# Optimization experiments

Measured on AMD Instinct MI355X. Metric: run time of the kernel, lower is better.

Reference implementation:

```python
import jax, jax.numpy as jnp
import numpy as np

D = 512      # feature dim d
N = 8192     # context length n
LMBD = 0.9   # eligibility trace decay


def _build_consts():
    two_d1 = 2 * D + 1
    # P: single nonzero entry at bottom-right
    P = np.zeros((two_d1, two_d1), dtype=np.float32)
    P[-1, -1] = 1.0
    # M: (n+1)x(n+1); top-left n x n block is lower-triangular lmbd^(row-col),
    # last row and last column are all zero (M[-1,-1] set to 0 in torch code)
    i = np.arange(N)
    diff = i[:, None] - i[None, :]
    Mnn = np.where(diff >= 0, LMBD ** np.maximum(diff, 0), 0.0).astype(np.float32)
    M = np.zeros((N + 1, N + 1), dtype=np.float32)
    M[:N, :N] = Mnn
    # Q: top-left 2d x 2d block = [[-I, I], [0, 0]]
    I = np.eye(D, dtype=np.float32)
    Q = np.zeros((two_d1, two_d1), dtype=np.float32)
    Q[:D, :D] = -I
    Q[:D, D:2 * D] = I
    return jnp.asarray(P), jnp.asarray(M), jnp.asarray(Q)


def setup_inputs() -> dict:
    key = jax.random.key(0)
    kz, = jax.random.split(key, 1)
    Z = jax.random.normal(kz, (2 * D + 1, N + 1), dtype=jnp.float32)
    alpha = jnp.ones((1,), dtype=jnp.float32)  # learned parameter
    P, M, Q = _build_consts()
    return {"Z": Z, "alpha": alpha, "P": P, "M": M, "Q": Q}


def reference(Z, alpha, P, M, Q):
    # Z: (2d+1, n+1). Matches torch: Z + alpha/n * P @ Z @ M @ Z.T @ Q @ Z
    n = Z.shape[1] - 1
    upd = ((((P @ Z) @ M) @ Z.T) @ Q) @ Z  # left-to-right like torch's @ chain
    return Z + (alpha[0] / n) * upd
```

## Files before the change

kernel.cpp:

```cpp
#include <hip/hip_runtime.h>

#define ND   512
#define NN   8192
#define NP1  8193

typedef float f4 __attribute__((ext_vector_type(4)));

#define NWB   512

__device__ __forceinline__ int sw(int j) { return j + (j >> 5); }
#define ZSLEN 8448

__global__ __launch_bounds__(256) void kW(const float* __restrict__ Z,
                                          float* __restrict__ w,
                                          float* __restrict__ out) {
    const int b = blockIdx.x;
    const int t = threadIdx.x;

    if (b < NWB) {
        __shared__ float zs[ZSLEN];
        __shared__ float es[256];
        __shared__ float red[4];
        const int c = b;
        const size_t base = (size_t)c * NP1;
        const int pre = (4 - (c & 3)) & 3;
        const int nq  = (NP1 - pre) >> 2;

        const f4* __restrict__ src = (const f4*)(Z + base + pre);
        f4* __restrict__ dst = (f4*)(out + base + pre);

        f4 xv[8];
#pragma unroll
        for (int m = 0; m < 8; ++m) {
            int i = t + 256 * m;
            xv[m] = (i < nq) ? src[i] : (f4){0.f, 0.f, 0.f, 0.f};
        }
#pragma unroll
        for (int m = 0; m < 8; ++m) {
            int i = t + 256 * m;
            if (i < nq) __builtin_nontemporal_store(xv[m], &dst[i]);
        }
#pragma unroll
        for (int m = 0; m < 8; ++m) {
            int i = t + 256 * m;
            if (i < nq) {
                int j = pre + 4 * i;
#pragma unroll
                for (int e = 0; e < 4; ++e)
                    if (j + e < NN) zs[sw(j + e)] = xv[m][e];
            }
        }
        if (t == 0) {
            for (int e = 0; e < pre; ++e) {
                float zv = Z[base + e];
                __builtin_nontemporal_store(zv, &out[base + e]);
                zs[sw(e)] = zv;
            }
            for (int j = pre + 4 * nq; j < NP1; ++j) {
                float zv = Z[base + j];
                __builtin_nontemporal_store(zv, &out[base + j]);
                if (j < NN) zs[sw(j)] = zv;
            }
        }
        __syncthreads();

        float r[32];
#pragma unroll
        for (int i = 0; i < 32; ++i) r[i] = zs[sw(32 * t + i)];

        const float L1 = 0.9f;
        float e = r[0];
#pragma unroll
        for (int i = 1; i < 32; ++i) e = fmaf(L1, e, r[i]);
        es[t] = e;
        __syncthreads();

        const float l2 = L1 * L1, l4v = l2 * l2, l8 = l4v * l4v;
        const float l16 = l8 * l8, lam32 = l16 * l16;
        float C = 0.f;
#pragma unroll
        for (int k = 7; k >= 1; --k) {
            float ek = (t - k >= 0) ? es[t - k] : 0.f;
            C = fmaf(lam32, C, ek);
        }

        float qv = C;
#pragma unroll
        for (int i = 0; i < 32; ++i) {
            qv = fmaf(L1, qv, r[i]);
            zs[sw(32 * t + i)] = qv;
        }
        __syncthreads();

        const f4* __restrict__ zrow4 = (const f4*)(Z + (size_t)(2 * ND) * NP1);
        float a0 = 0.f, a1 = 0.f, a2 = 0.f, a3 = 0.f;
#pragma unroll
        for (int m = 0; m < 8; ++m) {
            int i = t + 256 * m;
            f4 zv = zrow4[i];
            int j = 4 * i;
            a0 = fmaf(zv[0], zs[sw(j)],     a0);
            a1 = fmaf(zv[1], zs[sw(j + 1)], a1);
            a2 = fmaf(zv[2], zs[sw(j + 2)], a2);
            a3 = fmaf(zv[3], zs[sw(j + 3)], a3);
        }
        float acc = (a0 + a1) + (a2 + a3);

        for (int off = 32; off > 0; off >>= 1)
            acc += __shfl_down(acc, off, 64);
        if ((t & 63) == 0) red[t >> 6] = acc;
        __syncthreads();
        if (t == 0) w[c] = (red[0] + red[1]) + (red[2] + red[3]);
    } else {
        const size_t ZROW = (size_t)(2 * ND) * NP1;
        const f4* __restrict__ src = (const f4*)(Z + ZROW);
        f4* __restrict__ dst = (f4*)(out + ZROW);
        int i = (b - NWB) * 256 + t;
        dst[i] = src[i];
        if (b == NWB && t == 0) out[ZROW + NN] = Z[ZROW + NN];
    }
}

__global__ __launch_bounds__(256) void kU(const float* __restrict__ Z,
                                          const float* __restrict__ w,
                                          const float* __restrict__ alpha,
                                          float* __restrict__ out) {
    int j = blockIdx.x * 256 + threadIdx.x;
    if (j >= NP1) return;
    int c0 = blockIdx.y * 16;
    const size_t DS = (size_t)ND * NP1;
    float acc0 = 0.f, acc1 = 0.f;
#pragma unroll
    for (int cb = 0; cb < 16; cb += 4) {
        int c = c0 + cb;
        size_t base = (size_t)c * NP1 + (size_t)j;
        float lo0 = Z[base          ], lo1 = Z[base +     NP1];
        float lo2 = Z[base + 2 * NP1], lo3 = Z[base + 3 * NP1];
        float hi0 = Z[base + DS          ], hi1 = Z[base + DS +     NP1];
        float hi2 = Z[base + DS + 2 * NP1], hi3 = Z[base + DS + 3 * NP1];
        __builtin_nontemporal_store(hi0, &out[base + DS          ]);
        __builtin_nontemporal_store(hi1, &out[base + DS +     NP1]);
        __builtin_nontemporal_store(hi2, &out[base + DS + 2 * NP1]);
        __builtin_nontemporal_store(hi3, &out[base + DS + 3 * NP1]);
        acc0 = fmaf(w[c],     hi0 - lo0, acc0);
        acc1 = fmaf(w[c + 1], hi1 - lo1, acc1);
        acc0 = fmaf(w[c + 2], hi2 - lo2, acc0);
        acc1 = fmaf(w[c + 3], hi3 - lo3, acc1);
    }
    float s = alpha[0] * (1.0f / (float)NN);
    atomicAdd(&out[(size_t)(2 * ND) * NP1 + j], s * (acc0 + acc1));
}

extern "C" void kernel_launch(void* const* d_in, const int* in_sizes, int n_in,
                              void* d_out, int out_size, void* d_ws, size_t ws_size,
                              hipStream_t stream) {
    const float* Z     = (const float*)d_in[0];
    const float* alpha = (const float*)d_in[1];
    float* out = (float*)d_out;

    float* w = (float*)d_ws;

    kW<<<NWB + 8, 256, 0, stream>>>(Z, w, out);
    kU<<<dim3(33, 32), 256, 0, stream>>>(Z, w, alpha, out);
}
```

Measured before the change: 23.11 us.

## Split each row's decayed-scan into two half-row blocks with carry-in term

Each row's weighted prefix-scan dot product is now split across two blocks, each covering half the columns. This doubles the block count to 1024 and halves LDS use per block. The second-half block rebuilds the carry-in from the first half by summing the last 192 elements of that half with decay weights, truncating the geometric series. kU then adds the two partial weights per row. The changes should raise occupancy and parallelism in the first kernel, at the cost of a small approximation and some redundant reads.

```diff
diff --git a/kernel.cpp b/kernel.cpp
--- a/kernel.cpp
+++ b/kernel.cpp
@@ -6,103 +6,125 @@
 
 typedef float f4 __attribute__((ext_vector_type(4)));
 
-#define NWB   512
+#define NHB  1024
 
 __device__ __forceinline__ int sw(int j) { return j + (j >> 5); }
-#define ZSLEN 8448
+#define ZSLEN 4224
+
+#define LAM16 0.18530201888518410f
+#define L64   1.1790184577738583e-3f
+#define L128  1.3900845237714559e-6f
 
 __global__ __launch_bounds__(256) void kW(const float* __restrict__ Z,
-                                          float* __restrict__ w,
+                                          float* __restrict__ w2,
                                           float* __restrict__ out) {
     const int b = blockIdx.x;
     const int t = threadIdx.x;
 
-    if (b < NWB) {
+    if (b < NHB) {
         __shared__ float zs[ZSLEN];
         __shared__ float es[256];
         __shared__ float red[4];
-        const int c = b;
-        const size_t base = (size_t)c * NP1;
+        __shared__ float Esh;
+        const int c = b >> 1, h = b & 1;
+        const size_t rbase = (size_t)c * NP1;
+        const size_t cbase = rbase + (size_t)(4096 * h);
         const int pre = (4 - (c & 3)) & 3;
-        const int nq  = (NP1 - pre) >> 2;
+        const int ncols = h ? 4097 : 4096;
+        const int nq = (ncols - pre) >> 2;
 
-        const f4* __restrict__ src = (const f4*)(Z + base + pre);
-        f4* __restrict__ dst = (f4*)(out + base + pre);
+        const f4* __restrict__ src = (const f4*)(Z + cbase + pre);
+        f4* __restrict__ dst = (f4*)(out + cbase + pre);
 
-        f4 xv[8];
+        f4 xv[4];
 #pragma unroll
-        for (int m = 0; m < 8; ++m) {
+        for (int m = 0; m < 4; ++m) {
             int i = t + 256 * m;
             xv[m] = (i < nq) ? src[i] : (f4){0.f, 0.f, 0.f, 0.f};
         }
 #pragma unroll
-        for (int m = 0; m < 8; ++m) {
+        for (int m = 0; m < 4; ++m) {
             int i = t + 256 * m;
             if (i < nq) __builtin_nontemporal_store(xv[m], &dst[i]);
         }
 #pragma unroll
-        for (int m = 0; m < 8; ++m) {
+        for (int m = 0; m < 4; ++m) {
             int i = t + 256 * m;
             if (i < nq) {
-                int j = pre + 4 * i;
+                int L = pre + 4 * i;
 #pragma unroll
                 for (int e = 0; e < 4; ++e)
-                    if (j + e < NN) zs[sw(j + e)] = xv[m][e];
+                    if (L + e < 4096) zs[sw(L + e)] = xv[m][e];
             }
         }
         if (t == 0) {
             for (int e = 0; e < pre; ++e) {
-                float zv = Z[base + e];
-                __builtin_nontemporal_store(zv, &out[base + e]);
+                float zv = Z[cbase + e];
+                __builtin_nontemporal_store(zv, &out[cbase + e]);
                 zs[sw(e)] = zv;
             }
-            for (int j = pre + 4 * nq; j < NP1; ++j) {
-                float zv = Z[base + j];
-                __builtin_nontemporal_store(zv, &out[base + j]);
-                if (j < NN) zs[sw(j)] = zv;
+            for (int L = pre + 4 * nq; L < ncols; ++L) {
+                float zv = Z[cbase + L];
+                __builtin_nontemporal_store(zv, &out[cbase + L]);
+                if (L < 4096) zs[sw(L)] = zv;
             }
+            if (!h) Esh = 0.f;
+        }
+        if (h && t < 64) {
+            float za = Z[rbase + 4095 - t];
+            float zb = Z[rbase + 4031 - t];
+            float zc = Z[rbase + 3967 - t];
+            float p = 1.f;
+            if (t & 1)  p *= 0.9f;
+            if (t & 2)  p *= 0.81f;
+            if (t & 4)  p *= 0.6561f;
+            if (t & 8)  p *= 0.43046721f;
+            if (t & 16) p *= LAM16;
+            if (t & 32) p *= 0.03433683820292512f;
+            float term = p * fmaf(L64, zb, fmaf(L128, zc, za));
+            for (int off = 32; off > 0; off >>= 1)
+                term += __shfl_down(term, off, 64);
+            if (t == 0) Esh = term;
         }
         __syncthreads();
 
-        float r[32];
+        float r[16];
 #pragma unroll
-        for (int i = 0; i < 32; ++i) r[i] = zs[sw(32 * t + i)];
-
-        const float L1 = 0.9f;
+        for (int i = 0; i < 16; ++i) r[i] = zs[sw(16 * t + i)];
         float e = r[0];
 #pragma unroll
-        for (int i = 1; i < 32; ++i) e = fmaf(L1, e, r[i]);
+        for (int i = 1; i < 16; ++i) e = fmaf(0.9f, e, r[i]);
         es[t] = e;
         __syncthreads();
 
-        const float l2 = L1 * L1, l4v = l2 * l2, l8 = l4v * l4v;
-        const float l16 = l8 * l8, lam32 = l16 * l16;
         float C = 0.f;
 #pragma unroll
-        for (int k = 7; k >= 1; --k) {
-            float ek = (t - k >= 0) ? es[t - k] : 0.f;
-            C = fmaf(lam32, C, ek);
+        for (int k = 12; k >= 1; --k) {
+            int idx = t - k;
+            float ek = (idx >= 0) ? es[idx] : ((idx == -1) ? Esh : 0.f);
+            C = fmaf(LAM16, C, ek);
         }
 
         float qv = C;
 #pragma unroll
-        for (int i = 0; i < 32; ++i) {
-            qv = fmaf(L1, qv, r[i]);
-            zs[sw(32 * t + i)] = qv;
+        for (int i = 0; i < 16; ++i) {
+            qv = fmaf(0.9f, qv, r[i]);
+            zs[sw(16 * t + i)] = qv;
         }
         __syncthreads();
 
-        const f4* __restrict__ zrow4 = (const f4*)(Z + (size_t)(2 * ND) * NP1);
+        const f4* __restrict__ z4 =
+            (const f4*)(Z + (size_t)(2 * ND) * NP1 + (size_t)(4096 * h));
         float a0 = 0.f, a1 = 0.f, a2 = 0.f, a3 = 0.f;
 #pragma unroll
-        for (int m = 0; m < 8; ++m) {
+        for (int m = 0; m < 4; ++m) {
             int i = t + 256 * m;
-            f4 zv = zrow4[i];
-            int j = 4 * i;
-            a0 = fmaf(zv[0], zs[sw(j)],     a0);
-            a1 = fmaf(zv[1], zs[sw(j + 1)], a1);
-            a2 = fmaf(zv[2], zs[sw(j + 2)], a2);
-            a3 = fmaf(zv[3], zs[sw(j + 3)], a3);
+            f4 zz = z4[i];
+            int L = 4 * i;
+            a0 = fmaf(zz[0], zs[sw(L)],     a0);
+            a1 = fmaf(zz[1], zs[sw(L + 1)], a1);
+            a2 = fmaf(zz[2], zs[sw(L + 2)], a2);
+            a3 = fmaf(zz[3], zs[sw(L + 3)], a3);
         }
         float acc = (a0 + a1) + (a2 + a3);
 
@@ -110,19 +132,19 @@
             acc += __shfl_down(acc, off, 64);
         if ((t & 63) == 0) red[t >> 6] = acc;
         __syncthreads();
-        if (t == 0) w[c] = (red[0] + red[1]) + (red[2] + red[3]);
+        if (t == 0) w2[b] = (red[0] + red[1]) + (red[2] + red[3]);
     } else {
         const size_t ZROW = (size_t)(2 * ND) * NP1;
         const f4* __restrict__ src = (const f4*)(Z + ZROW);
         f4* __restrict__ dst = (f4*)(out + ZROW);
-        int i = (b - NWB) * 256 + t;
+        int i = (b - NHB) * 256 + t;
         dst[i] = src[i];
-        if (b == NWB && t == 0) out[ZROW + NN] = Z[ZROW + NN];
+        if (b == NHB && t == 0) out[ZROW + NN] = Z[ZROW + NN];
     }
 }
 
 __global__ __launch_bounds__(256) void kU(const float* __restrict__ Z,
-                                          const float* __restrict__ w,
+                                          const float* __restrict__ w2,
                                           const float* __restrict__ alpha,
                                           float* __restrict__ out) {
     int j = blockIdx.x * 256 + threadIdx.x;
@@ -133,6 +155,10 @@
 #pragma unroll
     for (int cb = 0; cb < 16; cb += 4) {
         int c = c0 + cb;
+        float ws0 = w2[2 * c    ] + w2[2 * c + 1];
+        float ws1 = w2[2 * c + 2] + w2[2 * c + 3];
+        float ws2 = w2[2 * c + 4] + w2[2 * c + 5];
+        float ws3 = w2[2 * c + 6] + w2[2 * c + 7];
         size_t base = (size_t)c * NP1 + (size_t)j;
         float lo0 = Z[base          ], lo1 = Z[base +     NP1];
         float lo2 = Z[base + 2 * NP1], lo3 = Z[base + 3 * NP1];
@@ -142,10 +168,10 @@
         __builtin_nontemporal_store(hi1, &out[base + DS +     NP1]);
         __builtin_nontemporal_store(hi2, &out[base + DS + 2 * NP1]);
         __builtin_nontemporal_store(hi3, &out[base + DS + 3 * NP1]);
-        acc0 = fmaf(w[c],     hi0 - lo0, acc0);
-        acc1 = fmaf(w[c + 1], hi1 - lo1, acc1);
-        acc0 = fmaf(w[c + 2], hi2 - lo2, acc0);
-        acc1 = fmaf(w[c + 3], hi3 - lo3, acc1);
+        acc0 = fmaf(ws0, hi0 - lo0, acc0);
+        acc1 = fmaf(ws1, hi1 - lo1, acc1);
+        acc0 = fmaf(ws2, hi2 - lo2, acc0);
+        acc1 = fmaf(ws3, hi3 - lo3, acc1);
     }
     float s = alpha[0] * (1.0f / (float)NN);
     atomicAdd(&out[(size_t)(2 * ND) * NP1 + j], s * (acc0 + acc1));
@@ -158,8 +184,8 @@
     const float* alpha = (const float*)d_in[1];
     float* out = (float*)d_out;
 
-    float* w = (float*)d_ws;
+    float* w2 = (float*)d_ws;
 
-    kW<<<NWB + 8, 256, 0, stream>>>(Z, w, out);
-    kU<<<dim3(33, 32), 256, 0, stream>>>(Z, w, alpha, out);
+    kW<<<NHB + 8, 256, 0, stream>>>(Z, w2, out);
+    kU<<<dim3(33, 32), 256, 0, stream>>>(Z, w2, alpha, out);
 }
```

Measured after the change: 24.46 us. 5.8% more time.
